# Optimization experiments

Hardware: AMD Instinct MI355X
Metric: run time of the kernel (lower is better)

The kernel has to match this reference:

```python
import jax, jax.numpy as jnp
import numpy as np

B, S, D = 4, 1024, 4096
HQ, HKV = 32, 8
HD = D // HQ          # 128
SCALE = HQ // HKV     # 4 (GQA repeat factor)


def setup_inputs() -> dict:
    key = jax.random.key(0)
    ks = jax.random.split(key, 11)
    s = 0.02  # init scale for weights
    return {
        "x": jax.random.normal(ks[0], (B, S, D), jnp.float32),
        # freqs_cis stored as (real, imag) pairs: [S, HD//2, 2]
        "freqs_cis": jax.random.normal(ks[1], (S, HD // 2, 2), jnp.float32),
        "Wq": jax.random.normal(ks[2], (D, HQ * HD), jnp.float32) * s,
        "bq": jnp.zeros((HQ * HD,), jnp.float32),
        "Wk": jax.random.normal(ks[3], (D, HKV * HD), jnp.float32) * s,
        "bk": jnp.zeros((HKV * HD,), jnp.float32),
        "Wv": jax.random.normal(ks[4], (D, HKV * HD), jnp.float32) * s,
        "bv": jnp.zeros((HKV * HD,), jnp.float32),
        "Wo": jax.random.normal(ks[5], (D, D), jnp.float32) * s,
        "bo": jnp.zeros((D,), jnp.float32),
        "startpos": 0,
    }


def _apply_rotary(x, fc):
    # x: [B, S, H, HD]; fc: [S, HD//2, 2] (real, imag)
    xr = x.reshape(*x.shape[:-1], HD // 2, 2)
    a, b = xr[..., 0], xr[..., 1]
    c = fc[None, :, None, :, 0]  # [1, S, 1, HD//2]
    d = fc[None, :, None, :, 1]
    # complex multiply (a+ib)*(c+id)
    out = jnp.stack([a * c - b * d, a * d + b * c], axis=-1)
    return out.reshape(x.shape)


def reference(x, freqs_cis, Wq, bq, Wk, bk, Wv, bv, Wo, bo, startpos):
    b, s, _ = x.shape
    q = (x @ Wq + bq).reshape(b, s, HQ, HD)
    k = (x @ Wk + bk).reshape(b, s, HKV, HD)
    v = (x @ Wv + bv).reshape(b, s, HKV, HD)

    fc = freqs_cis[startpos:startpos + s]
    q = _apply_rotary(q, fc)
    k = _apply_rotary(k, fc)

    # startpos == 0 and seq == cache_seq: cache write/read is identity
    q = q.transpose(0, 2, 1, 3)                            # [b, HQ, s, HD]
    k = jnp.repeat(k.transpose(0, 2, 1, 3), SCALE, axis=1)  # GQA repeat -> [b, HQ, s, HD]
    v = jnp.repeat(v.transpose(0, 2, 1, 3), SCALE, axis=1)

    scores = jnp.einsum('bhqd,bhkd->bhqk', q, k) / jnp.sqrt(jnp.float32(HD))
    causal = jnp.tril(jnp.ones((s, s), bool))
    scores = jnp.where(causal, scores, -jnp.inf)
    attn = jax.nn.softmax(scores, axis=-1)
    o = jnp.einsum('bhqk,bhkd->bhqd', attn, v)
    o = o.transpose(0, 2, 1, 3).reshape(b, s, HQ * HD)
    return o @ Wo + bo
```

## Files before the change

### kernel.cpp

```cpp
#include <hip/hip_runtime.h>
#include <hip/hip_bf16.h>

using bf16x8   = __attribute__((ext_vector_type(8))) __bf16;
using floatx4  = __attribute__((ext_vector_type(4))) float;
using floatx16 = __attribute__((ext_vector_type(16))) float;

#define DEVINL __device__ __forceinline__

DEVINL void gload16(const void* g, void* l) {
  __builtin_amdgcn_global_load_lds(
      (__attribute__((address_space(1))) void*)g,
      (__attribute__((address_space(3))) void*)l,
      16, 0, 0);
}

constexpr int S_ = 1024, D_ = 4096, HQ_ = 32, HKV_ = 8, HD_ = 128, B_ = 4;

__global__ void conv_bf16(const float* __restrict__ in, __bf16* __restrict__ out, int n) {
  int i = (blockIdx.x * 256 + threadIdx.x) * 8;
  if (i >= n) return;
  float4 a = *(const float4*)(in + i);
  float4 b = *(const float4*)(in + i + 4);
  bf16x8 o;
  o[0] = (__bf16)a.x; o[1] = (__bf16)a.y; o[2] = (__bf16)a.z; o[3] = (__bf16)a.w;
  o[4] = (__bf16)b.x; o[5] = (__bf16)b.y; o[6] = (__bf16)b.z; o[7] = (__bf16)b.w;
  *(bf16x8*)(out + i) = o;
}

__global__ void conv_transpose(const float* __restrict__ W, __bf16* __restrict__ WT, int K, int N) {
  __shared__ float tile[32][33];
  int n0 = blockIdx.x * 32, k0 = blockIdx.y * 32;
  int tx = threadIdx.x & 31, ty = threadIdx.x >> 5;
#pragma unroll
  for (int i = 0; i < 32; i += 8)
    tile[ty + i][tx] = W[(size_t)(k0 + ty + i) * N + n0 + tx];
  __syncthreads();
#pragma unroll
  for (int i = 0; i < 32; i += 8)
    WT[(size_t)(n0 + ty + i) * K + k0 + tx] = (__bf16)tile[tx][ty + i];
}

template<int MODE>
__global__ __launch_bounds__(512, 2)
void gemm8p(const __bf16* __restrict__ A, const __bf16* __restrict__ BT,
            const float* __restrict__ b0, const float* __restrict__ b1,
            const float* __restrict__ b2, void* __restrict__ Cout,
            int M, int N, int K)
{
  __shared__ __bf16 lds[65536];
  const int t = threadIdx.x;
  const int lane = t & 63, w = t >> 6;
  const int wm = w >> 2, wn = w & 3;
  const int g = (lane >> 4) & 3, c = lane & 15;

  const int gridX = gridDim.x;
  const int nwg = gridDim.x * gridDim.y;
  int lin = blockIdx.y * gridDim.x + blockIdx.x;
  lin = (lin & 7) * (nwg >> 3) + (lin >> 3);
  const int bx = lin % gridX, by = lin / gridX;
  const int m0 = by * 256, n0 = bx * 256;

  const floatx4 zero4 = {0.f, 0.f, 0.f, 0.f};
  floatx4 acc[2][2][4][2];
#pragma unroll
  for (int a = 0; a < 2; a++)
#pragma unroll
    for (int bq = 0; bq < 2; bq++)
#pragma unroll
      for (int i = 0; i < 4; i++)
#pragma unroll
        for (int j = 0; j < 2; j++) acc[a][bq][i][j] = zero4;

  const int t3 = t >> 3;
  const int l8 = ((t & 7) ^ (t3 & 7)) * 8;
  const int browc = (t3 & 31) + ((t3 >> 5) << 6);
  const __bf16* srcA0 = A  + (size_t)(m0 + t3) * K + l8;
  const __bf16* srcA1 = A  + (size_t)(m0 + 64 + t3) * K + l8;
  const __bf16* srcB0 = BT + (size_t)(n0 + browc) * K + l8;
  const __bf16* srcB1 = BT + (size_t)(n0 + 32 + browc) * K + l8;
  const size_t k128 = (size_t)128 * K;

  const int arow_rd = (wm * 64 + c) * 64;
  const int brow_rd = (wn * 32 + c) * 64;
  const int sel0 = ((g) ^ (c & 7)) * 8;
  const int sel1 = ((4 + g) ^ (c & 7)) * 8;

  const int NT = K >> 6;

#define STG(srcp, subofs, kt, pbuf)                                              \
  gload16((srcp) + (size_t)(kt) * 64,        &lds[(pbuf) + (subofs) + t * 8]);   \
  gload16((srcp) + (size_t)(kt) * 64 + k128, &lds[(pbuf) + (subofs) + 4096 + t * 8]);

#define LOADA(MQ, bb)                                                            \
  _Pragma("unroll")                                                              \
  for (int i = 0; i < 4; i++) {                                                  \
    af[i][0] = *(const bf16x8*)&lds[(bb) + (MQ)*8192 + arow_rd + i*1024 + sel0]; \
    af[i][1] = *(const bf16x8*)&lds[(bb) + (MQ)*8192 + arow_rd + i*1024 + sel1]; \
  }

#define LOADB(NQ, bb)                                                            \
  _Pragma("unroll")                                                              \
  for (int j = 0; j < 2; j++) {                                                  \
    bf[j][0] = *(const bf16x8*)&lds[(bb) + 16384 + (NQ)*8192 + brow_rd + j*1024 + sel0]; \
    bf[j][1] = *(const bf16x8*)&lds[(bb) + 16384 + (NQ)*8192 + brow_rd + j*1024 + sel1]; \
  }

#define MFMAQ(MQ, NQ)                                                            \
  __builtin_amdgcn_s_setprio(1);                                                 \
  _Pragma("unroll")                                                              \
  for (int i = 0; i < 4; i++)                                                    \
    _Pragma("unroll")                                                            \
    for (int j = 0; j < 2; j++) {                                                \
      acc[MQ][NQ][i][j] = __builtin_amdgcn_mfma_f32_16x16x32_bf16(af[i][0], bf[j][0], acc[MQ][NQ][i][j], 0, 0, 0); \
      acc[MQ][NQ][i][j] = __builtin_amdgcn_mfma_f32_16x16x32_bf16(af[i][1], bf[j][1], acc[MQ][NQ][i][j], 0, 0, 0); \
    }                                                                            \
  __builtin_amdgcn_s_setprio(0);                                                 \
  __builtin_amdgcn_sched_barrier(0);

#define BAR()                                                                    \
  __builtin_amdgcn_sched_barrier(0);                                             \
  __builtin_amdgcn_s_barrier();                                                  \
  __builtin_amdgcn_sched_barrier(0);

#define VMC(N) asm volatile("s_waitcnt vmcnt(" #N ")" ::: "memory");

#define TILE(v, DOSTAGE, VM0, VM1, VM2) {                                        \
  const int bb = ((v) & 1) * 32768;                                              \
  const int nb = bb ^ 32768;                                                     \
  bf16x8 af[4][2], bf[2][2];                                                     \
                                                                         \
  if (DOSTAGE) { STG(srcA0, 0, (v) + 1, nb) }                                    \
  VMC(VM0) BAR()                                                                 \
  LOADA(0, bb) LOADB(0, bb)                                                      \
  MFMAQ(0, 0)                                                                    \
                                                                         \
  if (DOSTAGE) { STG(srcB0, 16384, (v) + 1, nb) }                                \
  VMC(VM1) BAR()                                                                 \
  LOADB(1, bb)                                                                   \
  MFMAQ(0, 1)                                                                    \
                                                                         \
  if (DOSTAGE) { STG(srcB1, 24576, (v) + 1, nb) }                                \
  VMC(VM2) BAR()                                                                 \
  LOADA(1, bb)                                                                   \
  MFMAQ(1, 1)                                                                    \
                                                                         \
  if (DOSTAGE) { STG(srcA1, 8192, (v) + 1, nb) }                                 \
  BAR()                                                                          \
  LOADB(0, bb)                                                                   \
  MFMAQ(1, 0)                                                                    \
}

  STG(srcA0, 0, 0, 0)
  STG(srcB0, 16384, 0, 0)
  STG(srcB1, 24576, 0, 0)
  STG(srcA1, 8192, 0, 0)

  for (int v = 0; v < NT - 1; ++v) {
    TILE(v, true, 6, 6, 6)
  }
  TILE(NT - 1, false, 4, 2, 0)

#undef STG
#undef LOADA
#undef LOADB
#undef MFMAQ
#undef BAR
#undef VMC
#undef TILE

#pragma unroll
  for (int mq = 0; mq < 2; mq++)
#pragma unroll
    for (int nq = 0; nq < 2; nq++)
#pragma unroll
      for (int j = 0; j < 2; j++) {
        const int ncol = n0 + wn * 64 + nq * 32 + j * 16 + c;
#pragma unroll
        for (int i = 0; i < 4; i++) {
          const int mbase = m0 + wm * 128 + mq * 64 + i * 16 + g * 4;
#pragma unroll
          for (int r = 0; r < 4; r++) {
            const int m = mbase + r;
            float v = acc[mq][nq][i][j][r];
            if constexpr (MODE == 0) {
              ((float*)Cout)[(size_t)m * N + ncol] = v + b0[ncol];
            } else {
              const int bb2 = m >> 10, s = m & 1023;
              __bf16* qkv = (__bf16*)Cout;
              if (ncol < 4096) {
                v += b0[ncol];
                const int h = ncol >> 7, d = ncol & 127;
                qkv[(((size_t)bb2 * 32 + h) * 1024 + s) * 128 + d] = (__bf16)v;
              } else if (ncol < 5120) {
                const int nc = ncol - 4096;
                v += b1[nc];
                const int h = nc >> 7, d = nc & 127;
                qkv[16777216 + (((size_t)bb2 * 8 + h) * 1024 + s) * 128 + d] = (__bf16)v;
              } else {
                const int nc = ncol - 5120;
                v += b2[nc];
                const int h = nc >> 7, d = nc & 127;
                qkv[20971520 + (((size_t)bb2 * 8 + h) * 128 + d) * 1024 + s] = (__bf16)v;
              }
            }
          }
        }
      }
}

constexpr int NQCH = B_ * HQ_ * S_ * (HD_ / 8);
constexpr int NKCH = B_ * HKV_ * S_ * (HD_ / 8);
__global__ void rope_kernel(__bf16* __restrict__ qt, __bf16* __restrict__ kt,
                            const float* __restrict__ fc, const int* __restrict__ sp) {
  int tid = blockIdx.x * 256 + threadIdx.x;
  __bf16* p;
  int idx;
  if (tid < NQCH) { p = qt; idx = tid; }
  else { idx = tid - NQCH; if (idx >= NKCH) return; p = kt; }
  const int c8 = idx & 15;
  const int s  = (idx >> 4) & 1023;
  const int srow = sp[0] + s;
  const float* f = fc + (size_t)srow * 128 + c8 * 8;
  float4 fa = *(const float4*)(f);
  float4 fb = *(const float4*)(f + 4);
  __bf16* q = p + (size_t)idx * 8;
  bf16x8 v = *(const bf16x8*)q;
  float a0 = (float)v[0], b0 = (float)v[1], a1 = (float)v[2], b1 = (float)v[3];
  float a2 = (float)v[4], b2 = (float)v[5], a3 = (float)v[6], b3 = (float)v[7];
  bf16x8 o;
  o[0] = (__bf16)(a0 * fa.x - b0 * fa.y); o[1] = (__bf16)(a0 * fa.y + b0 * fa.x);
  o[2] = (__bf16)(a1 * fa.z - b1 * fa.w); o[3] = (__bf16)(a1 * fa.w + b1 * fa.z);
  o[4] = (__bf16)(a2 * fb.x - b2 * fb.y); o[5] = (__bf16)(a2 * fb.y + b2 * fb.x);
  o[6] = (__bf16)(a3 * fb.z - b3 * fb.w); o[7] = (__bf16)(a3 * fb.w + b3 * fb.z);
  *(bf16x8*)q = o;
}

__global__ __launch_bounds__(256, 2)
void flash_attn(const __bf16* __restrict__ qt, const __bf16* __restrict__ kt,
                const __bf16* __restrict__ vt, __bf16* __restrict__ obuf)
{
  const int lane = threadIdx.x & 63, w = threadIdx.x >> 6;
  const int rl = lane & 31, hi = lane >> 5;
  const int qb = blockIdx.x & 7;
  const int bh = blockIdx.x >> 3;
  const int b = bh >> 5, h = bh & 31, hk = h >> 2;
  const int q0w = (qb + w * 8) * 32;

  const __bf16* Qp = qt + (size_t)(b * HQ_ + h) * S_ * HD_;
  const __bf16* Kp = kt + (size_t)(b * HKV_ + hk) * S_ * HD_;
  const __bf16* Vp = vt + (size_t)(b * HKV_ + hk) * HD_ * S_;

  const __bf16* Qb = Qp + (size_t)(q0w + rl) * HD_ + hi * 8;
  bf16x8 qf[8];
#pragma unroll
  for (int d = 0; d < 8; d++) qf[d] = *(const bf16x8*)(Qb + d * 16);

  const __bf16* Kb = Kp + (size_t)rl * HD_ + hi * 8;
  const __bf16* Vb = Vp + (size_t)rl * S_ + hi * 8;

  const floatx16 zero16 = {0.f,0.f,0.f,0.f,0.f,0.f,0.f,0.f,0.f,0.f,0.f,0.f,0.f,0.f,0.f,0.f};
  floatx16 oacc[4];
#pragma unroll
  for (int dt = 0; dt < 4; dt++) oacc[dt] = zero16;

  float m_run = -__builtin_inff();
  float l_run = 0.f;
  const float ksc = 0.12751744875895f;

  for (int kv0 = 0; kv0 <= q0w; kv0 += 32) {
    floatx16 acc = zero16;
    bf16x8 kf[8];
#pragma unroll
    for (int d = 0; d < 8; d++)
      kf[d] = *(const bf16x8*)(Kb + (size_t)kv0 * HD_ + d * 16);
#pragma unroll
    for (int d = 0; d < 8; d++)
      acc = __builtin_amdgcn_mfma_f32_32x32x16_bf16(kf[d], qf[d], acc, 0, 0, 0);

    bf16x8 vf[4][2];
#pragma unroll
    for (int dt = 0; dt < 4; dt++)
#pragma unroll
      for (int kh = 0; kh < 2; kh++)
        vf[dt][kh] = *(const bf16x8*)(Vb + (size_t)dt * 32 * S_ + kv0 + kh * 16);

    if (kv0 == q0w) {
#pragma unroll
      for (int r = 0; r < 16; r++) {
        const int krel = (r & 3) + 8 * (r >> 2) + 4 * hi;
        if (krel > rl) acc[r] = -3e29f;
      }
    }

    float mx = acc[0];
#pragma unroll
    for (int r = 1; r < 16; r++) mx = fmaxf(mx, acc[r]);
    mx = fmaxf(mx, __shfl_xor(mx, 32));
    const float m_cand = mx * ksc;

    float m_use;
    const bool defer = __all(m_cand - m_run <= 8.0f);
    if (defer) {
      m_use = m_run;
    } else {
      const float m_new = fmaxf(m_run, m_cand);
      const float alpha = exp2f(m_run - m_new);
      l_run *= alpha;
      float ar[16];
#pragma unroll
      for (int r = 0; r < 16; r++)
        ar[r] = __shfl(alpha, (r & 3) + 8 * (r >> 2) + 4 * hi);
#pragma unroll
      for (int dt = 0; dt < 4; dt++)
#pragma unroll
        for (int r = 0; r < 16; r++) oacc[dt][r] *= ar[r];
      m_run = m_new;
      m_use = m_new;
    }

    float pr[16];
#pragma unroll
    for (int r = 0; r < 16; r++) pr[r] = exp2f(fmaf(acc[r], ksc, -m_use));
    float rs = pr[0];
#pragma unroll
    for (int r = 1; r < 16; r++) rs += pr[r];
    rs += __shfl_xor(rs, 32);
    l_run += rs;

    bf16x8 pa[2];
#pragma unroll
    for (int kh = 0; kh < 2; kh++) {
      const int rb = kh * 8;
      unsigned a0, b0, a1, b1;
      asm("v_cvt_pk_bf16_f32 %0, %1, %2" : "=v"(a0) : "v"(pr[rb + 0]), "v"(pr[rb + 1]));
      asm("v_cvt_pk_bf16_f32 %0, %1, %2" : "=v"(b0) : "v"(pr[rb + 4]), "v"(pr[rb + 5]));
      asm("v_cvt_pk_bf16_f32 %0, %1, %2" : "=v"(a1) : "v"(pr[rb + 2]), "v"(pr[rb + 3]));
      asm("v_cvt_pk_bf16_f32 %0, %1, %2" : "=v"(b1) : "v"(pr[rb + 6]), "v"(pr[rb + 7]));
      asm("v_permlane32_swap_b32 %0, %1" : "+v"(a0), "+v"(b0));
      asm("v_permlane32_swap_b32 %0, %1" : "+v"(a1), "+v"(b1));
      union { unsigned u[4]; bf16x8 v; } cvt;
      cvt.u[0] = a0; cvt.u[1] = a1; cvt.u[2] = b0; cvt.u[3] = b1;
      pa[kh] = cvt.v;
    }

#pragma unroll
    for (int dt = 0; dt < 4; dt++) {
      oacc[dt] = __builtin_amdgcn_mfma_f32_32x32x16_bf16(pa[0], vf[dt][0], oacc[dt], 0, 0, 0);
      oacc[dt] = __builtin_amdgcn_mfma_f32_32x32x16_bf16(pa[1], vf[dt][1], oacc[dt], 0, 0, 0);
    }
  }

  const float linv = 1.f / l_run;
  float lr[16];
#pragma unroll
  for (int r = 0; r < 16; r++)
    lr[r] = __shfl(linv, (r & 3) + 8 * (r >> 2) + 4 * hi);
#pragma unroll
  for (int dt = 0; dt < 4; dt++)
#pragma unroll
    for (int r = 0; r < 16; r++) {
      const int qrow = q0w + (r & 3) + 8 * (r >> 2) + 4 * hi;
      const size_t o = (size_t)(b * S_ + qrow) * D_ + h * HD_ + dt * 32 + rl;
      obuf[o] = (__bf16)(oacc[dt][r] * lr[r]);
    }
}

extern "C" void kernel_launch(void* const* d_in, const int* in_sizes, int n_in,
                              void* d_out, int out_size, void* d_ws, size_t ws_size,
                              hipStream_t stream) {
  (void)in_sizes; (void)n_in; (void)out_size;
  const float* x  = (const float*)d_in[0];
  const float* fc = (const float*)d_in[1];
  const float* Wq = (const float*)d_in[2];
  const float* bq = (const float*)d_in[3];
  const float* Wk = (const float*)d_in[4];
  const float* bk = (const float*)d_in[5];
  const float* Wv = (const float*)d_in[6];
  const float* bv = (const float*)d_in[7];
  const float* Wo = (const float*)d_in[8];
  const float* bo = (const float*)d_in[9];
  const int*   sp = (const int*)d_in[10];
  float* out = (float*)d_out;

  const size_t MB = 1024 * 1024;
  if (ws_size < 192 * MB) return;
  char* ws = (char*)d_ws;
  __bf16* xb     = (__bf16*)(ws + 0);
  __bf16* WqkvT  = (__bf16*)(ws + 32 * MB);
  __bf16* WoT    = (__bf16*)(ws + 80 * MB);
  __bf16* q_t    = (__bf16*)(ws + 112 * MB);
  __bf16* k_t    = (__bf16*)(ws + 144 * MB);
  __bf16* v_t    = (__bf16*)(ws + 152 * MB);
  __bf16* ob     = (__bf16*)(ws + 160 * MB);

  conv_bf16<<<8192, 256, 0, stream>>>(x, xb, D_ * B_ * S_);
  conv_transpose<<<dim3(128, 128), 256, 0, stream>>>(Wq, WqkvT, 4096, 4096);
  conv_transpose<<<dim3(32, 128),  256, 0, stream>>>(Wk, WqkvT + (size_t)4096 * 4096, 4096, 1024);
  conv_transpose<<<dim3(32, 128),  256, 0, stream>>>(Wv, WqkvT + (size_t)5120 * 4096, 4096, 1024);
  conv_transpose<<<dim3(128, 128), 256, 0, stream>>>(Wo, WoT, 4096, 4096);

  gemm8p<1><<<dim3(24, 16), 512, 0, stream>>>(xb, WqkvT, bq, bk, bv, q_t, 4096, 6144, 4096);

  rope_kernel<<<(NQCH + NKCH) / 256, 256, 0, stream>>>(q_t, k_t, fc, sp);
  flash_attn<<<1024, 256, 0, stream>>>(q_t, k_t, v_t, ob);

  gemm8p<0><<<dim3(16, 16), 512, 0, stream>>>(ob, WoT, bo, nullptr, nullptr, out, 4096, 4096, 4096);
}
```

Measured before the change: 617.8 us.

## Restructure GEMM main loop into ping-pong schedule with separate B fragment registers

Rewrites the bf16 GEMM inner loop so each phase issues LDS fragment reads and the next tile's global-to-LDS stage before a barrier, then runs MFMAs between barriers. It keeps two B fragment sets (bf0, bf1) so the last quadrant reuses bf0 instead of reloading it. Occupancy is lowered to one 512-thread block per CU to allow more registers. The aim is to overlap LDS reads and global loads with MFMA work more tightly. In exchange there are roughly twice as many barriers and fewer waves to hide latency.

New measurement: 613.0 us. No clear change (-0.8%).

```diff
diff --git a/kernel.cpp b/kernel.cpp
--- a/kernel.cpp
+++ b/kernel.cpp
@@ -41,7 +41,7 @@
 }
 
 template<int MODE>
-__global__ __launch_bounds__(512, 2)
+__global__ __launch_bounds__(512, 1)
 void gemm8p(const __bf16* __restrict__ A, const __bf16* __restrict__ BT,
             const float* __restrict__ b0, const float* __restrict__ b1,
             const float* __restrict__ b2, void* __restrict__ Cout,
@@ -87,6 +87,8 @@
 
   const int NT = K >> 6;
 
+  bf16x8 af[4][2], bf0[2][2], bf1[2][2];
+
 #define STG(srcp, subofs, kt, pbuf)                                              \
   gload16((srcp) + (size_t)(kt) * 64,        &lds[(pbuf) + (subofs) + t * 8]);   \
   gload16((srcp) + (size_t)(kt) * 64 + k128, &lds[(pbuf) + (subofs) + 4096 + t * 8]);
@@ -98,75 +100,84 @@
     af[i][1] = *(const bf16x8*)&lds[(bb) + (MQ)*8192 + arow_rd + i*1024 + sel1]; \
   }
 
-#define LOADB(NQ, bb)                                                            \
+#define LOADB(DST, NQ, bb)                                                       \
   _Pragma("unroll")                                                              \
   for (int j = 0; j < 2; j++) {                                                  \
-    bf[j][0] = *(const bf16x8*)&lds[(bb) + 16384 + (NQ)*8192 + brow_rd + j*1024 + sel0]; \
-    bf[j][1] = *(const bf16x8*)&lds[(bb) + 16384 + (NQ)*8192 + brow_rd + j*1024 + sel1]; \
+    DST[j][0] = *(const bf16x8*)&lds[(bb) + 16384 + (NQ)*8192 + brow_rd + j*1024 + sel0]; \
+    DST[j][1] = *(const bf16x8*)&lds[(bb) + 16384 + (NQ)*8192 + brow_rd + j*1024 + sel1]; \
   }
 
-#define MFMAQ(MQ, NQ)                                                            \
+#define MFMAQ(MQ, NQ, BF)                                                        \
   __builtin_amdgcn_s_setprio(1);                                                 \
   _Pragma("unroll")                                                              \
   for (int i = 0; i < 4; i++)                                                    \
     _Pragma("unroll")                                                            \
     for (int j = 0; j < 2; j++) {                                                \
-      acc[MQ][NQ][i][j] = __builtin_amdgcn_mfma_f32_16x16x32_bf16(af[i][0], bf[j][0], acc[MQ][NQ][i][j], 0, 0, 0); \
-      acc[MQ][NQ][i][j] = __builtin_amdgcn_mfma_f32_16x16x32_bf16(af[i][1], bf[j][1], acc[MQ][NQ][i][j], 0, 0, 0); \
+      acc[MQ][NQ][i][j] = __builtin_amdgcn_mfma_f32_16x16x32_bf16(af[i][0], BF[j][0], acc[MQ][NQ][i][j], 0, 0, 0); \
+      acc[MQ][NQ][i][j] = __builtin_amdgcn_mfma_f32_16x16x32_bf16(af[i][1], BF[j][1], acc[MQ][NQ][i][j], 0, 0, 0); \
     }                                                                            \
-  __builtin_amdgcn_s_setprio(0);                                                 \
-  __builtin_amdgcn_sched_barrier(0);
-
-#define BAR()                                                                    \
-  __builtin_amdgcn_sched_barrier(0);                                             \
-  __builtin_amdgcn_s_barrier();                                                  \
-  __builtin_amdgcn_sched_barrier(0);
-
+  __builtin_amdgcn_s_setprio(0);
+
+#define SBAR() __builtin_amdgcn_sched_barrier(0)
+#define BARR() __builtin_amdgcn_s_barrier()
 #define VMC(N) asm volatile("s_waitcnt vmcnt(" #N ")" ::: "memory");
-
-#define TILE(v, DOSTAGE, VM0, VM1, VM2) {                                        \
-  const int bb = ((v) & 1) * 32768;                                              \
-  const int nb = bb ^ 32768;                                                     \
-  bf16x8 af[4][2], bf[2][2];                                                     \
-                                                                         \
-  if (DOSTAGE) { STG(srcA0, 0, (v) + 1, nb) }                                    \
-  VMC(VM0) BAR()                                                                 \
-  LOADA(0, bb) LOADB(0, bb)                                                      \
-  MFMAQ(0, 0)                                                                    \
-                                                                         \
-  if (DOSTAGE) { STG(srcB0, 16384, (v) + 1, nb) }                                \
-  VMC(VM1) BAR()                                                                 \
-  LOADB(1, bb)                                                                   \
-  MFMAQ(0, 1)                                                                    \
-                                                                         \
-  if (DOSTAGE) { STG(srcB1, 24576, (v) + 1, nb) }                                \
-  VMC(VM2) BAR()                                                                 \
-  LOADA(1, bb)                                                                   \
-  MFMAQ(1, 1)                                                                    \
-                                                                         \
-  if (DOSTAGE) { STG(srcA1, 8192, (v) + 1, nb) }                                 \
-  BAR()                                                                          \
-  LOADB(0, bb)                                                                   \
-  MFMAQ(1, 0)                                                                    \
-}
+#define LGKM0() asm volatile("s_waitcnt lgkmcnt(0)" ::: "memory");
 
   STG(srcA0, 0, 0, 0)
   STG(srcB0, 16384, 0, 0)
   STG(srcB1, 24576, 0, 0)
   STG(srcA1, 8192, 0, 0)
+  VMC(4) BARR(); SBAR();
 
   for (int v = 0; v < NT - 1; ++v) {
-    TILE(v, true, 6, 6, 6)
+    const int bb = (v & 1) * 32768;
+    const int nb = bb ^ 32768;
+    LOADA(0, bb)
+    LOADB(bf0, 0, bb)
+    STG(srcA0, 0, v + 1, nb)
+    SBAR(); VMC(4) BARR(); LGKM0() SBAR();
+    MFMAQ(0, 0, bf0)
+    SBAR(); BARR(); SBAR();
+    LOADB(bf1, 1, bb)
+    STG(srcB0, 16384, v + 1, nb)
+    SBAR(); VMC(4) BARR(); LGKM0() SBAR();
+    MFMAQ(0, 1, bf1)
+    SBAR(); BARR(); SBAR();
+    LOADA(1, bb)
+    STG(srcB1, 24576, v + 1, nb)
+    SBAR(); BARR(); LGKM0() SBAR();
+    MFMAQ(1, 1, bf1)
+    SBAR(); BARR(); SBAR();
+    STG(srcA1, 8192, v + 1, nb)
+    SBAR(); VMC(4) BARR(); SBAR();
+    MFMAQ(1, 0, bf0)
+    SBAR(); BARR(); SBAR();
   }
-  TILE(NT - 1, false, 4, 2, 0)
+  {
+    const int bb = ((NT - 1) & 1) * 32768;
+    LOADA(0, bb)
+    LOADB(bf0, 0, bb)
+    SBAR(); VMC(2) BARR(); LGKM0() SBAR();
+    MFMAQ(0, 0, bf0)
+    SBAR(); BARR(); SBAR();
+    LOADB(bf1, 1, bb)
+    SBAR(); VMC(0) BARR(); LGKM0() SBAR();
+    MFMAQ(0, 1, bf1)
+    SBAR(); BARR(); SBAR();
+    LOADA(1, bb)
+    SBAR(); BARR(); LGKM0() SBAR();
+    MFMAQ(1, 1, bf1)
+    MFMAQ(1, 0, bf0)
+  }
 
 #undef STG
 #undef LOADA
 #undef LOADB
 #undef MFMAQ
-#undef BAR
+#undef SBAR
+#undef BARR
 #undef VMC
-#undef TILE
+#undef LGKM0
 
 #pragma unroll
   for (int mq = 0; mq < 2; mq++)
```
